# Kernel tuning notes

Hardware: AMD Instinct MI355X
Metric: run time of the kernel (lower is better)

## Reference

```python
import jax, jax.numpy as jnp
import numpy as np

N = 100000   # nodes
E = 1600000  # edges
D = 64       # hidden_channels == out_channels
L = 3        # num_layers
EPS = 1e-5
SCALE = 1.0 / float(np.sqrt(D))


def setup_inputs() -> dict:
    key = jax.random.key(0)
    ks = jax.random.split(key, 12)
    x = jax.random.normal(ks[0], (N, D), dtype=jnp.float32)
    edge_index = jax.random.randint(ks[1], (2, E), 0, N, dtype=jnp.int32)
    s = 0.1
    Wq = jax.random.normal(ks[2], (L, D, D), dtype=jnp.float32) * s
    Wk = jax.random.normal(ks[3], (L, D, D), dtype=jnp.float32) * s
    Wv = jax.random.normal(ks[4], (L, D, D), dtype=jnp.float32) * s
    Ws = jax.random.normal(ks[5], (L, D, D), dtype=jnp.float32) * s
    bq = jax.random.normal(ks[6], (L, D), dtype=jnp.float32) * s
    bk = jax.random.normal(ks[7], (L, D), dtype=jnp.float32) * s
    bv = jax.random.normal(ks[8], (L, D), dtype=jnp.float32) * s
    bs = jax.random.normal(ks[9], (L, D), dtype=jnp.float32) * s
    gamma = jnp.ones((L, D), dtype=jnp.float32)
    beta = jnp.zeros((L, D), dtype=jnp.float32)
    return {"x": x, "edge_index": edge_index, "Wq": Wq, "bq": bq,
            "Wk": Wk, "bk": bk, "Wv": Wv, "bv": bv, "Ws": Ws, "bs": bs,
            "gamma": gamma, "beta": beta}


def layer_norm(h, g, b):
    mu = h.mean(-1, keepdims=True)
    var = ((h - mu) ** 2).mean(-1, keepdims=True)
    return (h - mu) * jax.lax.rsqrt(var + EPS) * g + b


def transformer_conv(x, src, dst, Wq, bq, Wk, bk, Wv, bv, Ws, bs):
    # PyG TransformerConv, heads=1, concat=True, root_weight=True, beta=False
    q = x @ Wq + bq            # [N, D]
    k = x @ Wk + bk            # [N, D]
    v = x @ Wv + bv            # [N, D]
    # per-edge attention logit: <q_dst, k_src> / sqrt(D)
    score = jnp.einsum('ed,ed->e', q[dst], k[src]) * SCALE  # [E]
    # segment softmax over incoming edges of each dst node
    m = jax.ops.segment_max(score, dst, num_segments=N)     # [N]
    e = jnp.exp(score - m[dst])                             # [E]
    denom = jax.ops.segment_sum(e, dst, num_segments=N)     # [N]
    alpha = e / denom[dst]                                  # [E]
    agg = jax.ops.segment_sum(alpha[:, None] * v[src], dst, num_segments=N)  # [N, D]
    return agg + x @ Ws + bs   # root/skip connection


def reference(x, edge_index, Wq, bq, Wk, bk, Wv, bv, Ws, bs, gamma, beta):
    src, dst = edge_index[0], edge_index[1]
    x_init = None
    for i in range(L):
        h = transformer_conv(x, src, dst, Wq[i], bq[i], Wk[i], bk[i],
                             Wv[i], bv[i], Ws[i], bs[i])
        h = jax.nn.relu(h)
        if i == 0:
            x_init = h
        else:
            h = h + x_init
        x = layer_norm(h, gamma[i], beta[i])
    return x
```

## Files before the change

kernel.cpp:

```cpp
#include <hip/hip_runtime.h>
#include <math.h>

#define NN 100000
#define EE 1600000
#define EPS 1e-5f
#define SCALEF 0.125f

#define NB 1024
#define BCAP 2688
#define CH 4096

typedef __attribute__((ext_vector_type(4))) float f32x4;
typedef __attribute__((ext_vector_type(8))) short bf16x8;
typedef __attribute__((ext_vector_type(8))) unsigned short u16x8;

__device__ __forceinline__ unsigned short f2bf_rne(float f) {
    unsigned u = __builtin_bit_cast(unsigned, f);
    u += 0x7FFFu + ((u >> 16) & 1u);
    return (unsigned short)(u >> 16);
}
__device__ __forceinline__ float bf2f(unsigned short h) {
    return __builtin_bit_cast(float, ((unsigned)h) << 16);
}


__global__ __launch_bounds__(256) void bin_edges2(const int* __restrict__ ei,
                                                  int* __restrict__ bcnt,
                                                  unsigned* __restrict__ bbuf, int E) {
    __shared__ int hist[NB];
    __shared__ int gbase[NB];
    __shared__ int cur[NB];
    int base = blockIdx.x * CH;
    int tid = threadIdx.x;

    for (int i = tid; i < NB; i += 256) { hist[i] = 0; cur[i] = 0; }
    __syncthreads();

    for (int i = tid; i < CH; i += 256) {
        int e = base + i;
        if (e < E) atomicAdd(&hist[ei[E + e] >> 7], 1);
    }
    __syncthreads();

    for (int i = tid; i < NB; i += 256)
        gbase[i] = hist[i] ? atomicAdd(&bcnt[i], hist[i]) : 0;
    __syncthreads();

    for (int i = tid; i < CH; i += 256) {
        int e = base + i;
        if (e < E) {
            int s = ei[e];
            int d = ei[E + e];
            int b = d >> 7;
            int pos = gbase[b] + atomicAdd(&cur[b], 1);
            if (pos < BCAP) bbuf[b * BCAP + pos] = ((unsigned)s << 7) | (unsigned)(d & 127);
        }
    }
}

__global__ __launch_bounds__(1024) void scan_buckets(const int* __restrict__ bcnt,
                                                     int* __restrict__ bbase) {
    __shared__ int sh[1024];
    int tid = threadIdx.x;
    int v = bcnt[tid];
    sh[tid] = v;
    __syncthreads();
    for (int off = 1; off < 1024; off <<= 1) {
        int t = (tid >= off) ? sh[tid - off] : 0;
        __syncthreads();
        sh[tid] += t;
        __syncthreads();
    }
    bbase[tid] = sh[tid] - v;
}

__global__ __launch_bounds__(256) void bucket_csr(const unsigned* __restrict__ bbuf,
                                                  const int* __restrict__ bcnt,
                                                  const int* __restrict__ bbase,
                                                  int* __restrict__ iOff,
                                                  int* __restrict__ csr, int N) {
    __shared__ unsigned ed[BCAP];
    __shared__ int hist[128], excl[128], cur[128];
    int b = blockIdx.x;
    int tid = threadIdx.x;
    int cnt = min(bcnt[b], BCAP);
    int base = bbase[b];

    for (int i = tid; i < cnt; i += 256) ed[i] = bbuf[b * BCAP + i];
    if (tid < 128) { hist[tid] = 0; cur[tid] = 0; }
    __syncthreads();
    for (int i = tid; i < cnt; i += 256) atomicAdd(&hist[ed[i] & 127], 1);
    __syncthreads();
    if (tid < 128) excl[tid] = hist[tid];
    __syncthreads();
    for (int off = 1; off < 128; off <<= 1) {
        int t = (tid < 128 && tid >= off) ? excl[tid - off] : 0;
        __syncthreads();
        if (tid < 128) excl[tid] += t;
        __syncthreads();
    }
    if (tid < 128) {
        int ex = excl[tid] - hist[tid];
        excl[tid] = ex;
        int node = b * 128 + tid;
        if (node <= N) iOff[node] = base + ex;
    }
    __syncthreads();
    for (int i = tid; i < cnt; i += 256) {
        unsigned pk = ed[i];
        int ld = pk & 127;
        int pos = atomicAdd(&cur[ld], 1);
        csr[base + excl[ld] + pos] = (int)(pk >> 7);
    }
}


__global__ __launch_bounds__(64) void wfrag_prep(
    const float* __restrict__ Wq, const float* __restrict__ Wk,
    const float* __restrict__ Wv, const float* __restrict__ Ws,
    unsigned short* __restrict__ fragH, unsigned short* __restrict__ fragL)
{
    int bm = blockIdx.x;
    int layer = bm >> 2, m = bm & 3;
    const float* W = ((m == 0) ? Wq : (m == 1) ? Wk : (m == 2) ? Wv : Ws) + layer * 4096;
    int l = threadIdx.x;
    int colb = l & 15, kg = l >> 4;
#pragma unroll
    for (int ks = 0; ks < 2; ks++)
#pragma unroll
        for (int ct = 0; ct < 4; ct++) {
            size_t base = ((((size_t)bm * 2 + ks) * 4 + ct) * 64 + l) * 8;
#pragma unroll
            for (int e = 0; e < 8; e++) {
                int kk = ks * 32 + kg * 8 + e;
                int col = ct * 16 + colb;
                float f = W[kk * 64 + col];
                unsigned short h = f2bf_rne(f);
                fragH[base + e] = h;
                fragL[base + e] = f2bf_rne(f - bf2f(h));
            }
        }
}


__global__ __launch_bounds__(256) void gemm4_mfma(const void* __restrict__ xp, int xbf, int N,
    const unsigned short* __restrict__ fragH, const unsigned short* __restrict__ fragL,
    int layer,
    const float* __restrict__ bq, const float* __restrict__ bk,
    const float* __restrict__ bv, const float* __restrict__ bs,
    unsigned short* __restrict__ oq, unsigned char* __restrict__ kv8,
    float* __restrict__ sc, unsigned short* __restrict__ os)
{
    __shared__ unsigned short xhi[64][80];
    __shared__ unsigned short xlo[64][80];

    int tid = threadIdx.x;
    int row0 = blockIdx.x * 64;

    if (xbf) {
        const unsigned short* xb = (const unsigned short*)xp;
#pragma unroll
        for (int i = 0; i < 2; i++) {
            int idx = tid + i * 256;
            int r = idx >> 3;
            int c8 = (idx & 7) * 8;
            u16x8 u = {0, 0, 0, 0, 0, 0, 0, 0};
            if (row0 + r < N) u = *(const u16x8*)&xb[(size_t)(row0 + r) * 64 + c8];
            *(u16x8*)&xhi[r][c8] = u;
        }
    } else {
        const float* xf = (const float*)xp;
#pragma unroll
        for (int i = 0; i < 4; i++) {
            int idx = tid + i * 256;
            int r = idx >> 4;
            int c4 = (idx & 15) * 4;
            f32x4 f = {0.f, 0.f, 0.f, 0.f};
            if (row0 + r < N) f = *(const f32x4*)&xf[(size_t)(row0 + r) * 64 + c4];
            ushort4 hh, ll;
            unsigned short h;
            h = f2bf_rne(f.x); hh.x = h; ll.x = f2bf_rne(f.x - bf2f(h));
            h = f2bf_rne(f.y); hh.y = h; ll.y = f2bf_rne(f.y - bf2f(h));
            h = f2bf_rne(f.z); hh.z = h; ll.z = f2bf_rne(f.z - bf2f(h));
            h = f2bf_rne(f.w); hh.w = h; ll.w = f2bf_rne(f.w - bf2f(h));
            *(ushort4*)&xhi[r][c4] = hh;
            *(ushort4*)&xlo[r][c4] = ll;
        }
    }
    __syncthreads();

    int w = tid >> 6, l = tid & 63;
    int colb = l & 15, kg = l >> 4;
    int bm = layer * 4 + w;
    const float* bias = (w == 0) ? bq : (w == 1) ? bk : (w == 2) ? bv : bs;

    bf16x8 bh[2][4], bl[2][4];
#pragma unroll
    for (int ks = 0; ks < 2; ks++)
#pragma unroll
        for (int ct = 0; ct < 4; ct++) {
            size_t fb = ((((size_t)bm * 2 + ks) * 4 + ct) * 64 + l) * 8;
            bh[ks][ct] = *(const bf16x8*)&fragH[fb];
            bl[ks][ct] = *(const bf16x8*)&fragL[fb];
        }

    f32x4 acc[4][4] = {};
#pragma unroll
    for (int rt = 0; rt < 4; rt++) {
        int r = rt * 16 + colb;
#pragma unroll
        for (int ks = 0; ks < 2; ks++) {
            bf16x8 ah = *(const bf16x8*)&xhi[r][ks * 32 + kg * 8];
#pragma unroll
            for (int ct = 0; ct < 4; ct++) {
                acc[rt][ct] = __builtin_amdgcn_mfma_f32_16x16x32_bf16(ah, bh[ks][ct], acc[rt][ct], 0, 0, 0);
                acc[rt][ct] = __builtin_amdgcn_mfma_f32_16x16x32_bf16(ah, bl[ks][ct], acc[rt][ct], 0, 0, 0);
            }
            if (!xbf) {
                bf16x8 al = *(const bf16x8*)&xlo[r][ks * 32 + kg * 8];
#pragma unroll
                for (int ct = 0; ct < 4; ct++)
                    acc[rt][ct] = __builtin_amdgcn_mfma_f32_16x16x32_bf16(al, bh[ks][ct], acc[rt][ct], 0, 0, 0);
            }
        }
    }

    float bias4[4];
#pragma unroll
    for (int ct = 0; ct < 4; ct++) bias4[ct] = bias[ct * 16 + colb];
#pragma unroll
    for (int rt = 0; rt < 4; rt++)
#pragma unroll
        for (int ct = 0; ct < 4; ct++)
#pragma unroll
            for (int j = 0; j < 4; j++) acc[rt][ct][j] += bias4[ct];

    if (w == 0 || w == 3) {
        unsigned short* dst = (w == 0) ? oq : os;
#pragma unroll
        for (int rt = 0; rt < 4; rt++)
#pragma unroll
            for (int j = 0; j < 4; j++) {
                int gr = row0 + rt * 16 + kg * 4 + j;
                if (gr < N) {
                    ushort4 pk;
                    pk.x = f2bf_rne(acc[rt][0][j]);
                    pk.y = f2bf_rne(acc[rt][1][j]);
                    pk.z = f2bf_rne(acc[rt][2][j]);
                    pk.w = f2bf_rne(acc[rt][3][j]);
                    *(ushort4*)&dst[(size_t)gr * 64 + colb * 4] = pk;
                }
            }
    } else {
        int voff = (w == 2) ? 4 : 0;
#pragma unroll
        for (int rt = 0; rt < 4; rt++)
#pragma unroll
            for (int j = 0; j < 4; j++) {
                int gr = row0 + rt * 16 + kg * 4 + j;
                float a0 = acc[rt][0][j], a1 = acc[rt][1][j];
                float a2 = acc[rt][2][j], a3 = acc[rt][3][j];
                float m = fmaxf(fmaxf(fabsf(a0), fabsf(a1)), fmaxf(fabsf(a2), fabsf(a3)));
                m = fmaxf(m, __shfl_xor(m, 1));
                m = fmaxf(m, __shfl_xor(m, 2));
                m = fmaxf(m, __shfl_xor(m, 4));
                m = fmaxf(m, __shfl_xor(m, 8));
                float rs = 127.f / fmaxf(m, 1e-20f);
                unsigned pk;
                pk  = (unsigned)((int)rintf(a0 * rs) + 128);
                pk |= (unsigned)((int)rintf(a1 * rs) + 128) << 8;
                pk |= (unsigned)((int)rintf(a2 * rs) + 128) << 16;
                pk |= (unsigned)((int)rintf(a3 * rs) + 128) << 24;
                if (gr < N) {
                    *(unsigned*)(kv8 + (size_t)gr * 128 + colb * 8 + voff) = pk;
                    if (colb == 0) sc[gr * 2 + (w == 2 ? 1 : 0)] = m * (1.f / 127.f);
                }
            }
    }
}


__global__ __launch_bounds__(256) void node_attn(
    const int* __restrict__ off, const int* __restrict__ csr,
    const unsigned short* __restrict__ q, const unsigned char* __restrict__ kv8,
    const float* __restrict__ sc, const unsigned short* __restrict__ xs,
    const float* __restrict__ gamma, const float* __restrict__ beta,
    unsigned short* __restrict__ xinit, unsigned short* __restrict__ xoutb,
    float* __restrict__ outf, int layer, int N)
{
    int node = (blockIdx.x * blockDim.x + threadIdx.x) >> 4;
    int sl = threadIdx.x & 15;
    if (node >= N) return;
    int e0 = off[node], e1 = off[node + 1];
    size_t nb = (size_t)node * 64 + sl * 4;

    ushort4 qu = *(const ushort4*)&q[nb];
    const float SC2 = SCALEF * 1.44269504f;
    f32x4 qv;
    qv.x = bf2f(qu.x) * SC2; qv.y = bf2f(qu.y) * SC2;
    qv.z = bf2f(qu.z) * SC2; qv.w = bf2f(qu.w) * SC2;
    float sq = qv.x + qv.y + qv.z + qv.w;
    sq += __shfl_xor(sq, 1); sq += __shfl_xor(sq, 2);
    sq += __shfl_xor(sq, 4); sq += __shfl_xor(sq, 8);
    float b128 = 128.f * sq;

    float ssum = 0.f, s128 = 0.f;
    f32x4 acc = {0.f, 0.f, 0.f, 0.f};

#define EDGE(ks, vs, ku, vu)                                                \
    {                                                                       \
        float t = qv.x * (float)(ku & 0xffu) +                              \
                  qv.y * (float)((ku >> 8) & 0xffu) +                       \
                  qv.z * (float)((ku >> 16) & 0xffu) +                      \
                  qv.w * (float)(ku >> 24);                                 \
        t += __shfl_xor(t, 1); t += __shfl_xor(t, 2);                       \
        t += __shfl_xor(t, 4); t += __shfl_xor(t, 8);                       \
        float d = (t - b128) * ks;                                          \
        float p = __builtin_amdgcn_exp2f(d);                                \
        ssum += p;                                                          \
        float pp = p * vs;                                                  \
        s128 += pp;                                                         \
        acc.x += pp * (float)(vu & 0xffu);                                  \
        acc.y += pp * (float)((vu >> 8) & 0xffu);                           \
        acc.z += pp * (float)((vu >> 16) & 0xffu);                          \
        acc.w += pp * (float)(vu >> 24);                                    \
    }

    int e = e0;
    for (; e + 3 < e1; e += 4) {
        int s0 = csr[e + 0], s1 = csr[e + 1], s2 = csr[e + 2], s3 = csr[e + 3];
        float2 c0 = *(const float2*)&sc[s0 * 2];
        float2 c1 = *(const float2*)&sc[s1 * 2];
        float2 c2 = *(const float2*)&sc[s2 * 2];
        float2 c3 = *(const float2*)&sc[s3 * 2];
        uint2 u0 = *(const uint2*)(kv8 + (size_t)s0 * 128 + sl * 8);
        uint2 u1 = *(const uint2*)(kv8 + (size_t)s1 * 128 + sl * 8);
        uint2 u2 = *(const uint2*)(kv8 + (size_t)s2 * 128 + sl * 8);
        uint2 u3 = *(const uint2*)(kv8 + (size_t)s3 * 128 + sl * 8);
        EDGE(c0.x, c0.y, u0.x, u0.y);
        EDGE(c1.x, c1.y, u1.x, u1.y);
        EDGE(c2.x, c2.y, u2.x, u2.y);
        EDGE(c3.x, c3.y, u3.x, u3.y);
    }
    for (; e < e1; e++) {
        int s0 = csr[e];
        float2 c0 = *(const float2*)&sc[s0 * 2];
        uint2 u0 = *(const uint2*)(kv8 + (size_t)s0 * 128 + sl * 8);
        EDGE(c0.x, c0.y, u0.x, u0.y);
    }

    float inv = (e1 > e0) ? 1.f / ssum : 0.f;
    float corr = 128.f * s128;
    ushort4 sku = *(const ushort4*)&xs[nb];
    f32x4 h;
    h.x = fmaxf((acc.x - corr) * inv + bf2f(sku.x), 0.f);
    h.y = fmaxf((acc.y - corr) * inv + bf2f(sku.y), 0.f);
    h.z = fmaxf((acc.z - corr) * inv + bf2f(sku.z), 0.f);
    h.w = fmaxf((acc.w - corr) * inv + bf2f(sku.w), 0.f);
    if (layer == 0) {
        ushort4 hu;
        hu.x = f2bf_rne(h.x); hu.y = f2bf_rne(h.y);
        hu.z = f2bf_rne(h.z); hu.w = f2bf_rne(h.w);
        *(ushort4*)&xinit[nb] = hu;
    } else {
        ushort4 xi = *(const ushort4*)&xinit[nb];
        h.x += bf2f(xi.x); h.y += bf2f(xi.y);
        h.z += bf2f(xi.z); h.w += bf2f(xi.w);
    }

    float s1 = h.x + h.y + h.z + h.w;
    s1 += __shfl_xor(s1, 1); s1 += __shfl_xor(s1, 2);
    s1 += __shfl_xor(s1, 4); s1 += __shfl_xor(s1, 8);
    float mu = s1 * (1.f / 64.f);
    f32x4 d;
    d.x = h.x - mu; d.y = h.y - mu; d.z = h.z - mu; d.w = h.w - mu;
    float s2 = d.x * d.x + d.y * d.y + d.z * d.z + d.w * d.w;
    s2 += __shfl_xor(s2, 1); s2 += __shfl_xor(s2, 2);
    s2 += __shfl_xor(s2, 4); s2 += __shfl_xor(s2, 8);
    float rs = rsqrtf(s2 * (1.f / 64.f) + EPS);
    f32x4 g4, bb;
    g4.x = gamma[sl];      g4.y = gamma[sl + 16];
    g4.z = gamma[sl + 32]; g4.w = gamma[sl + 48];
    bb.x = beta[sl];       bb.y = beta[sl + 16];
    bb.z = beta[sl + 32];  bb.w = beta[sl + 48];
    f32x4 o;
    o.x = d.x * rs * g4.x + bb.x;
    o.y = d.y * rs * g4.y + bb.y;
    o.z = d.z * rs * g4.z + bb.z;
    o.w = d.w * rs * g4.w + bb.w;
    size_t nb0 = (size_t)node * 64;
    if (layer == 2) {
        outf[nb0 + sl]      = o.x;
        outf[nb0 + sl + 16] = o.y;
        outf[nb0 + sl + 32] = o.z;
        outf[nb0 + sl + 48] = o.w;
    } else {
        xoutb[nb0 + sl]      = f2bf_rne(o.x);
        xoutb[nb0 + sl + 16] = f2bf_rne(o.y);
        xoutb[nb0 + sl + 32] = f2bf_rne(o.z);
        xoutb[nb0 + sl + 48] = f2bf_rne(o.w);
    }
}


extern "C" void kernel_launch(void* const* d_in, const int* in_sizes, int n_in,
                              void* d_out, int out_size, void* d_ws, size_t ws_size,
                              hipStream_t stream) {
    const float* x     = (const float*)d_in[0];
    const int*   ei    = (const int*)d_in[1];
    const float* Wq    = (const float*)d_in[2];
    const float* bq    = (const float*)d_in[3];
    const float* Wk    = (const float*)d_in[4];
    const float* bk    = (const float*)d_in[5];
    const float* Wv    = (const float*)d_in[6];
    const float* bv    = (const float*)d_in[7];
    const float* Wsk   = (const float*)d_in[8];
    const float* bsk   = (const float*)d_in[9];
    const float* gamma = (const float*)d_in[10];
    const float* beta  = (const float*)d_in[11];
    float* out = (float*)d_out;

    const int N = NN, E = EE;
    const size_t ND = (size_t)N * 64;

    char* p = (char*)d_ws;
    unsigned short* fQ  = (unsigned short*)p; p += ND * 2;
    unsigned short* fS  = (unsigned short*)p; p += ND * 2;
    unsigned short* fI  = (unsigned short*)p; p += ND * 2;
    unsigned char*  fKV = (unsigned char*)p;  p += ND * 2;
    float* fSC = (float*)p; p += (size_t)N * 2 * 4;
    int* iOff = (int*)p;  p += (size_t)(N + 1) * 4;
    int* bcnt = (int*)p;  p += NB * 4;
    int* bbase = (int*)p; p += NB * 4;
    int* iSrc = (int*)p;  p += (size_t)E * 4;
    unsigned short* fragH = (unsigned short*)p; p += (size_t)12 * 2 * 4 * 64 * 8 * 2;
    unsigned short* fragL = (unsigned short*)p; p += (size_t)12 * 2 * 4 * 64 * 8 * 2;
    unsigned* bbuf = (unsigned*)fS;

    hipMemsetAsync(bcnt, 0, NB * 4, stream);
    bin_edges2<<<(E + CH - 1) / CH, 256, 0, stream>>>(ei, bcnt, bbuf, E);
    wfrag_prep<<<12, 64, 0, stream>>>(Wq, Wk, Wv, Wsk, fragH, fragL);
    scan_buckets<<<1, 1024, 0, stream>>>(bcnt, bbase);
    bucket_csr<<<NB, 256, 0, stream>>>(bbuf, bcnt, bbase, iOff, iSrc, N);

    for (int l = 0; l < 3; l++) {
        const void* xin = (l == 0) ? (const void*)x : (const void*)fQ;
        gemm4_mfma<<<(N + 63) / 64, 256, 0, stream>>>(xin, (l == 0) ? 0 : 1, N,
            fragH, fragL, l,
            bq + l * 64, bk + l * 64, bv + l * 64, bsk + l * 64,
            fQ, fKV, fSC, fS);
        node_attn<<<(N * 16 + 255) / 256, 256, 0, stream>>>(iOff, iSrc, fQ, fKV, fSC, fS,
            gamma + l * 64, beta + l * 64, fI, fQ, out, l, N);
    }
}
```

Baseline: 298.2 us.

## Use signed int8 dot4 for attention scores with 8 lanes per node

Keys are now stored as signed int8 in a separate half of the row, and the query is quantized to int8 per node inside node_attn, so the score dot product uses the hardware sdot4 instruction instead of float unpack-and-multiply. Each node is now handled by 8 lanes with 8 dims each instead of 16 lanes with 4, which cuts the shuffle-reduction depth and doubles per-lane work. The KV layout changes from interleaved K/V to K in bytes 0-63 and V in bytes 64-127. The int8 query quantization adds approximation error to the attention logits.

```diff
diff --git a/kernel.cpp b/kernel.cpp
--- a/kernel.cpp
+++ b/kernel.cpp
@@ -21,6 +21,17 @@
 }
 __device__ __forceinline__ float bf2f(unsigned short h) {
     return __builtin_bit_cast(float, ((unsigned)h) << 16);
+}
+__device__ __forceinline__ int dot4(int a, int b, int c) {
+#if __has_builtin(__builtin_amdgcn_sdot4)
+    return __builtin_amdgcn_sdot4(a, b, c, false);
+#else
+    int r = c;
+#pragma unroll
+    for (int i = 0; i < 4; i++)
+        r += ((int)(char)(a >> (8 * i)) & ~0) * ((int)(char)(b >> (8 * i)));
+    return r;
+#endif
 }
 
 
@@ -251,8 +262,7 @@
                     *(ushort4*)&dst[(size_t)gr * 64 + colb * 4] = pk;
                 }
             }
-    } else {
-        int voff = (w == 2) ? 4 : 0;
+    } else if (w == 1) {
 #pragma unroll
         for (int rt = 0; rt < 4; rt++)
 #pragma unroll
@@ -265,15 +275,41 @@
                 m = fmaxf(m, __shfl_xor(m, 2));
                 m = fmaxf(m, __shfl_xor(m, 4));
                 m = fmaxf(m, __shfl_xor(m, 8));
-                float rs = 127.f / fmaxf(m, 1e-20f);
+                m = fmaxf(m, 1e-20f);
+                float rs = 127.f / m;
+                unsigned pk;
+                pk  = (unsigned)((int)rintf(a0 * rs) & 0xff);
+                pk |= (unsigned)((int)rintf(a1 * rs) & 0xff) << 8;
+                pk |= (unsigned)((int)rintf(a2 * rs) & 0xff) << 16;
+                pk |= (unsigned)((int)rintf(a3 * rs) & 0xff) << 24;
+                if (gr < N) {
+                    *(unsigned*)(kv8 + (size_t)gr * 128 + colb * 4) = pk;
+                    if (colb == 0) sc[gr * 2] = m * (1.f / 127.f);
+                }
+            }
+    } else {
+#pragma unroll
+        for (int rt = 0; rt < 4; rt++)
+#pragma unroll
+            for (int j = 0; j < 4; j++) {
+                int gr = row0 + rt * 16 + kg * 4 + j;
+                float a0 = acc[rt][0][j], a1 = acc[rt][1][j];
+                float a2 = acc[rt][2][j], a3 = acc[rt][3][j];
+                float m = fmaxf(fmaxf(fabsf(a0), fabsf(a1)), fmaxf(fabsf(a2), fabsf(a3)));
+                m = fmaxf(m, __shfl_xor(m, 1));
+                m = fmaxf(m, __shfl_xor(m, 2));
+                m = fmaxf(m, __shfl_xor(m, 4));
+                m = fmaxf(m, __shfl_xor(m, 8));
+                m = fmaxf(m, 1e-20f);
+                float rs = 127.f / m;
                 unsigned pk;
                 pk  = (unsigned)((int)rintf(a0 * rs) + 128);
                 pk |= (unsigned)((int)rintf(a1 * rs) + 128) << 8;
                 pk |= (unsigned)((int)rintf(a2 * rs) + 128) << 16;
                 pk |= (unsigned)((int)rintf(a3 * rs) + 128) << 24;
                 if (gr < N) {
-                    *(unsigned*)(kv8 + (size_t)gr * 128 + colb * 8 + voff) = pk;
-                    if (colb == 0) sc[gr * 2 + (w == 2 ? 1 : 0)] = m * (1.f / 127.f);
+                    *(unsigned*)(kv8 + (size_t)gr * 128 + 64 + colb * 4) = pk;
+                    if (colb == 0) sc[gr * 2 + 1] = m * (1.f / 127.f);
                 }
             }
     }
@@ -288,117 +324,136 @@
     unsigned short* __restrict__ xinit, unsigned short* __restrict__ xoutb,
     float* __restrict__ outf, int layer, int N)
 {
-    int node = (blockIdx.x * blockDim.x + threadIdx.x) >> 4;
-    int sl = threadIdx.x & 15;
+    int node = (blockIdx.x * blockDim.x + threadIdx.x) >> 3;
+    int sl = threadIdx.x & 7;
     if (node >= N) return;
     int e0 = off[node], e1 = off[node + 1];
-    size_t nb = (size_t)node * 64 + sl * 4;
-
-    ushort4 qu = *(const ushort4*)&q[nb];
-    const float SC2 = SCALEF * 1.44269504f;
-    f32x4 qv;
-    qv.x = bf2f(qu.x) * SC2; qv.y = bf2f(qu.y) * SC2;
-    qv.z = bf2f(qu.z) * SC2; qv.w = bf2f(qu.w) * SC2;
-    float sq = qv.x + qv.y + qv.z + qv.w;
-    sq += __shfl_xor(sq, 1); sq += __shfl_xor(sq, 2);
-    sq += __shfl_xor(sq, 4); sq += __shfl_xor(sq, 8);
-    float b128 = 128.f * sq;
+    size_t nb = (size_t)node * 64 + sl * 8;
+
+    u16x8 qu = *(const u16x8*)&q[nb];
+    float qf[8];
+#pragma unroll
+    for (int i = 0; i < 8; i++) qf[i] = bf2f((unsigned short)qu[i]);
+    float am = 0.f;
+#pragma unroll
+    for (int i = 0; i < 8; i++) am = fmaxf(am, fabsf(qf[i]));
+    am = fmaxf(am, __shfl_xor(am, 1));
+    am = fmaxf(am, __shfl_xor(am, 2));
+    am = fmaxf(am, __shfl_xor(am, 4));
+    am = fmaxf(am, 1e-20f);
+    float qrs = 127.f / am;
+    unsigned qlo = 0, qhi = 0;
+#pragma unroll
+    for (int i = 0; i < 4; i++)
+        qlo |= (unsigned)((int)rintf(qf[i] * qrs) & 0xff) << (8 * i);
+#pragma unroll
+    for (int i = 0; i < 4; i++)
+        qhi |= (unsigned)((int)rintf(qf[4 + i] * qrs) & 0xff) << (8 * i);
+    const float qC = am * (1.f / 127.f) * SCALEF * 1.44269504f;
 
     float ssum = 0.f, s128 = 0.f;
-    f32x4 acc = {0.f, 0.f, 0.f, 0.f};
-
-#define EDGE(ks, vs, ku, vu)                                                \
+    float a0 = 0.f, a1 = 0.f, a2 = 0.f, a3 = 0.f;
+    float a4 = 0.f, a5 = 0.f, a6 = 0.f, a7 = 0.f;
+
+#define EDGE(ks, vs, kk, vv)                                                \
     {                                                                       \
-        float t = qv.x * (float)(ku & 0xffu) +                              \
-                  qv.y * (float)((ku >> 8) & 0xffu) +                       \
-                  qv.z * (float)((ku >> 16) & 0xffu) +                      \
-                  qv.w * (float)(ku >> 24);                                 \
-        t += __shfl_xor(t, 1); t += __shfl_xor(t, 2);                       \
-        t += __shfl_xor(t, 4); t += __shfl_xor(t, 8);                       \
-        float d = (t - b128) * ks;                                          \
+        int t = dot4((int)kk.y, (int)qhi, dot4((int)kk.x, (int)qlo, 0));    \
+        t += __shfl_xor(t, 1); t += __shfl_xor(t, 2); t += __shfl_xor(t, 4);\
+        float d = (float)t * ks * qC;                                       \
         float p = __builtin_amdgcn_exp2f(d);                                \
         ssum += p;                                                          \
         float pp = p * vs;                                                  \
         s128 += pp;                                                         \
-        acc.x += pp * (float)(vu & 0xffu);                                  \
-        acc.y += pp * (float)((vu >> 8) & 0xffu);                           \
-        acc.z += pp * (float)((vu >> 16) & 0xffu);                          \
-        acc.w += pp * (float)(vu >> 24);                                    \
+        a0 += pp * (float)(vv.x & 0xffu);                                   \
+        a1 += pp * (float)((vv.x >> 8) & 0xffu);                            \
+        a2 += pp * (float)((vv.x >> 16) & 0xffu);                           \
+        a3 += pp * (float)(vv.x >> 24);                                     \
+        a4 += pp * (float)(vv.y & 0xffu);                                   \
+        a5 += pp * (float)((vv.y >> 8) & 0xffu);                            \
+        a6 += pp * (float)((vv.y >> 16) & 0xffu);                           \
+        a7 += pp * (float)(vv.y >> 24);                                     \
     }
 
     int e = e0;
     for (; e + 3 < e1; e += 4) {
         int s0 = csr[e + 0], s1 = csr[e + 1], s2 = csr[e + 2], s3 = csr[e + 3];
+        const unsigned char* r0 = kv8 + (size_t)s0 * 128 + sl * 8;
+        const unsigned char* r1 = kv8 + (size_t)s1 * 128 + sl * 8;
+        const unsigned char* r2 = kv8 + (size_t)s2 * 128 + sl * 8;
+        const unsigned char* r3 = kv8 + (size_t)s3 * 128 + sl * 8;
+        uint2 k0 = *(const uint2*)r0, v0 = *(const uint2*)(r0 + 64);
+        uint2 k1 = *(const uint2*)r1, v1 = *(const uint2*)(r1 + 64);
+        uint2 k2 = *(const uint2*)r2, v2 = *(const uint2*)(r2 + 64);
+        uint2 k3 = *(const uint2*)r3, v3 = *(const uint2*)(r3 + 64);
         float2 c0 = *(const float2*)&sc[s0 * 2];
         float2 c1 = *(const float2*)&sc[s1 * 2];
         float2 c2 = *(const float2*)&sc[s2 * 2];
         float2 c3 = *(const float2*)&sc[s3 * 2];
-        uint2 u0 = *(const uint2*)(kv8 + (size_t)s0 * 128 + sl * 8);
-        uint2 u1 = *(const uint2*)(kv8 + (size_t)s1 * 128 + sl * 8);
-        uint2 u2 = *(const uint2*)(kv8 + (size_t)s2 * 128 + sl * 8);
-        uint2 u3 = *(const uint2*)(kv8 + (size_t)s3 * 128 + sl * 8);
-        EDGE(c0.x, c0.y, u0.x, u0.y);
-        EDGE(c1.x, c1.y, u1.x, u1.y);
-        EDGE(c2.x, c2.y, u2.x, u2.y);
-        EDGE(c3.x, c3.y, u3.x, u3.y);
+        EDGE(c0.x, c0.y, k0, v0);
+        EDGE(c1.x, c1.y, k1, v1);
+        EDGE(c2.x, c2.y, k2, v2);
+        EDGE(c3.x, c3.y, k3, v3);
     }
     for (; e < e1; e++) {
         int s0 = csr[e];
+        const unsigned char* r0 = kv8 + (size_t)s0 * 128 + sl * 8;
+        uint2 k0 = *(const uint2*)r0, v0 = *(const uint2*)(r0 + 64);
         float2 c0 = *(const float2*)&sc[s0 * 2];
-        uint2 u0 = *(const uint2*)(kv8 + (size_t)s0 * 128 + sl * 8);
-        EDGE(c0.x, c0.y, u0.x, u0.y);
+        EDGE(c0.x, c0.y, k0, v0);
     }
 
     float inv = (e1 > e0) ? 1.f / ssum : 0.f;
     float corr = 128.f * s128;
-    ushort4 sku = *(const ushort4*)&xs[nb];
-    f32x4 h;
-    h.x = fmaxf((acc.x - corr) * inv + bf2f(sku.x), 0.f);
-    h.y = fmaxf((acc.y - corr) * inv + bf2f(sku.y), 0.f);
-    h.z = fmaxf((acc.z - corr) * inv + bf2f(sku.z), 0.f);
-    h.w = fmaxf((acc.w - corr) * inv + bf2f(sku.w), 0.f);
+    u16x8 sku = *(const u16x8*)&xs[nb];
+    float h[8];
+    h[0] = fmaxf((a0 - corr) * inv + bf2f((unsigned short)sku[0]), 0.f);
+    h[1] = fmaxf((a1 - corr) * inv + bf2f((unsigned short)sku[1]), 0.f);
+    h[2] = fmaxf((a2 - corr) * inv + bf2f((unsigned short)sku[2]), 0.f);
+    h[3] = fmaxf((a3 - corr) * inv + bf2f((unsigned short)sku[3]), 0.f);
+    h[4] = fmaxf((a4 - corr) * inv + bf2f((unsigned short)sku[4]), 0.f);
+    h[5] = fmaxf((a5 - corr) * inv + bf2f((unsigned short)sku[5]), 0.f);
+    h[6] = fmaxf((a6 - corr) * inv + bf2f((unsigned short)sku[6]), 0.f);
+    h[7] = fmaxf((a7 - corr) * inv + bf2f((unsigned short)sku[7]), 0.f);
+
     if (layer == 0) {
-        ushort4 hu;
-        hu.x = f2bf_rne(h.x); hu.y = f2bf_rne(h.y);
-        hu.z = f2bf_rne(h.z); hu.w = f2bf_rne(h.w);
-        *(ushort4*)&xinit[nb] = hu;
+        u16x8 hu;
+#pragma unroll
+        for (int i = 0; i < 8; i++) hu[i] = (short)f2bf_rne(h[i]);
+        *(u16x8*)&xinit[nb] = hu;
     } else {
-        ushort4 xi = *(const ushort4*)&xinit[nb];
-        h.x += bf2f(xi.x); h.y += bf2f(xi.y);
-        h.z += bf2f(xi.z); h.w += bf2f(xi.w);
-    }
-
-    float s1 = h.x + h.y + h.z + h.w;
-    s1 += __shfl_xor(s1, 1); s1 += __shfl_xor(s1, 2);
-    s1 += __shfl_xor(s1, 4); s1 += __shfl_xor(s1, 8);
+        u16x8 xi = *(const u16x8*)&xinit[nb];
+#pragma unroll
+        for (int i = 0; i < 8; i++) h[i] += bf2f((unsigned short)xi[i]);
+    }
+
+    float s1 = 0.f;
+#pragma unroll
+    for (int i = 0; i < 8; i++) s1 += h[i];
+    s1 += __shfl_xor(s1, 1); s1 += __shfl_xor(s1, 2); s1 += __shfl_xor(s1, 4);
     float mu = s1 * (1.f / 64.f);
-    f32x4 d;
-    d.x = h.x - mu; d.y = h.y - mu; d.z = h.z - mu; d.w = h.w - mu;
-    float s2 = d.x * d.x + d.y * d.y + d.z * d.z + d.w * d.w;
-    s2 += __shfl_xor(s2, 1); s2 += __shfl_xor(s2, 2);
-    s2 += __shfl_xor(s2, 4); s2 += __shfl_xor(s2, 8);
+    float dd[8], s2 = 0.f;
+#pragma unroll
+    for (int i = 0; i < 8; i++) { dd[i] = h[i] - mu; s2 += dd[i] * dd[i]; }
+    s2 += __shfl_xor(s2, 1); s2 += __shfl_xor(s2, 2); s2 += __shfl_xor(s2, 4);
     float rs = rsqrtf(s2 * (1.f / 64.f) + EPS);
-    f32x4 g4, bb;
-    g4.x = gamma[sl];      g4.y = gamma[sl + 16];
-    g4.z = gamma[sl + 32]; g4.w = gamma[sl + 48];
-    bb.x = beta[sl];       bb.y = beta[sl + 16];
-    bb.z = beta[sl + 32];  bb.w = beta[sl + 48];
-    f32x4 o;
-    o.x = d.x * rs * g4.x + bb.x;
-    o.y = d.y * rs * g4.y + bb.y;
-    o.z = d.z * rs * g4.z + bb.z;
-    o.w = d.w * rs * g4.w + bb.w;
+
     size_t nb0 = (size_t)node * 64;
-    if (layer == 2) {
-        outf[nb0 + sl]      = o.x;
-        outf[nb0 + sl + 16] = o.y;
-        outf[nb0 + sl + 32] = o.z;
-        outf[nb0 + sl + 48] = o.w;
-    } else {
-        xoutb[nb0 + sl]      = f2bf_rne(o.x);
-        xoutb[nb0 + sl + 16] = f2bf_rne(o.y);
-        xoutb[nb0 + sl + 32] = f2bf_rne(o.z);
-        xoutb[nb0 + sl + 48] = f2bf_rne(o.w);
+#pragma unroll
+    for (int j = 0; j < 4; j++) {
+        int dim = 16 * j + 2 * sl;
+        float2 g2 = *(const float2*)&gamma[dim];
+        float2 b2 = *(const float2*)&beta[dim];
+        float olo = dd[j] * rs * g2.x + b2.x;
+        float ohi = dd[4 + j] * rs * g2.y + b2.y;
+        if (layer == 2) {
+            float2 o2 = {olo, ohi};
+            *(float2*)&outf[nb0 + dim] = o2;
+        } else {
+            ushort2 o2;
+            o2.x = f2bf_rne(olo);
+            o2.y = f2bf_rne(ohi);
+            *(ushort2*)&xoutb[nb0 + dim] = o2;
+        }
     }
 }
 
@@ -449,7 +504,7 @@
             fragH, fragL, l,
             bq + l * 64, bk + l * 64, bv + l * 64, bsk + l * 64,
             fQ, fKV, fSC, fS);
-        node_attn<<<(N * 16 + 255) / 256, 256, 0, stream>>>(iOff, iSrc, fQ, fKV, fSC, fS,
+        node_attn<<<(N * 8 + 255) / 256, 256, 0, stream>>>(iOff, iSrc, fQ, fKV, fSC, fS,
             gamma + l * 64, beta + l * 64, fI, fQ, out, l, N);
     }
 }
```

After: 286.8 us. 3.8% less time.
